# Kernel tuning notes

Measured on AMD Instinct MI355X. Metric: run time of the kernel, lower is better.

The kernel has to match this reference:

```python
import jax, jax.numpy as jnp
from jax import lax
import numpy as np

# 6D tensors: (N, C, h1, w1, h2, w2); weights: (Cout, Cin, k,k,k,k)
DN = lax.ConvDimensionNumbers(lhs_spec=(0, 1, 2, 3, 4, 5),
                              rhs_spec=(0, 1, 2, 3, 4, 5),
                              out_spec=(0, 1, 2, 3, 4, 5))


def conv4d_relu(x, w, b):
    # true 4D convolution, stride 1, SAME padding, then bias + ReLU
    y = lax.conv_general_dilated(x, w, window_strides=(1, 1, 1, 1),
                                 padding='SAME', dimension_numbers=DN)
    return jax.nn.relu(y + b.reshape(1, -1, 1, 1, 1, 1))


def _perm(x):
    # swap the two (h, w) spatial pairs of the correlation tensor
    return jnp.transpose(x, (0, 1, 4, 5, 2, 3))


def _sym(x, w, b):
    # symmetric_mode branch: f(x) + perm(f(perm(x)))
    return conv4d_relu(x, w, b) + _perm(conv4d_relu(_perm(x), w, b))


def setup_inputs() -> dict:
    key = jax.random.key(0)
    ks = jax.random.split(key, 9)
    B, S = 4, 20
    sc = 0.05
    return {
        'x':    jax.random.normal(ks[0], (B, 1, S, S, S, S), dtype=jnp.float32),
        'w0':   jax.random.normal(ks[1], (16, 1, 5, 5, 5, 5), dtype=jnp.float32) * sc,
        'b0':   jax.random.normal(ks[2], (16,), dtype=jnp.float32) * sc,
        'w10':  jax.random.normal(ks[3], (8, 16, 3, 3, 5, 5), dtype=jnp.float32) * sc,
        'b10':  jax.random.normal(ks[4], (8,), dtype=jnp.float32) * sc,
        'w11':  jax.random.normal(ks[5], (8, 16, 5, 5, 5, 5), dtype=jnp.float32) * sc,
        'b11':  jax.random.normal(ks[6], (8,), dtype=jnp.float32) * sc,
        'w2':   jax.random.normal(ks[7], (1, 16, 5, 5, 5, 5), dtype=jnp.float32) * sc,
        'b2':   jax.random.normal(ks[8], (1,), dtype=jnp.float32) * sc,
    }


def reference(x, w0, b0, w10, b10, w11, b11, w2, b2):
    x = _sym(x, w0, b0)                       # [B,16,S,S,S,S]
    x0 = _sym(x, w10, b10)                    # [B, 8,S,S,S,S]
    x1 = _sym(x, w11, b11)                    # [B, 8,S,S,S,S]
    x = jnp.concatenate((x0, x1), axis=1)     # [B,16,S,S,S,S]
    return _sym(x, w2, b2)                    # [B, 1,S,S,S,S]
```

## Files before the change

### kernel.cpp

```cpp
#include <hip/hip_runtime.h>

#define TS 20
#define TS2 400

typedef __attribute__((ext_vector_type(8))) __bf16 bf16x8;
typedef __attribute__((ext_vector_type(4))) __bf16 bf16x4;
typedef __attribute__((ext_vector_type(4))) float  f32x4;
typedef __attribute__((ext_vector_type(4))) int    int4v;

__device__ __forceinline__ float relu_f(float v) { return v > 0.0f ? v : 0.0f; }

#define MFMA16(a, b, c) __builtin_amdgcn_mfma_f32_16x16x32_bf16((a), (b), (c), 0, 0, 0)

#define LPAD 580

__global__ __launch_bounds__(256)
void pack_w0(const float* __restrict__ w0, __bf16* __restrict__ wpk0)
{
    int idx = blockIdx.x * 256 + (int)threadIdx.x;
    if (idx >= 25 * 32 * 32) return;
    const int c = idx & 31;
    const int m = (idx >> 5) & 31;
    const int e = idx >> 10;
    float v = 0.0f;
    if (c < 25) {
        const int co = m & 15;
        const int k1o = c / 5, k2o = c % 5, k3i = e / 5, k4i = e % 5;
        if (m < 16) v = w0[co * 625 + k1o * 125 + k2o * 25 + k3i * 5 + k4i];
        else        v = w0[co * 625 + k3i * 125 + k4i * 25 + k1o * 5 + k2o];
    }
    wpk0[idx] = (__bf16)v;
}

__global__ __launch_bounds__(256)
void pack_wmid(const float* __restrict__ w10, const float* __restrict__ w11,
               __bf16* __restrict__ wpk)
{
    int idx = blockIdx.x * 256 + (int)threadIdx.x;
    if (idx >= 650 * 512) return;
    const int ci  = idx & 15;
    const int m   = (idx >> 4) & 31;
    const int off = idx >> 9;
    const int inner = off % 26, outer = off / 26;
    const int d1 = outer / 5 - 2, d2 = outer % 5 - 2;
    float v = 0.0f;
    if (inner < 25) {
        const int d3 = inner / 5 - 2, d4 = inner % 5 - 2;
        const int co = m & 7;
        const bool isB  = (m & 8)  != 0;
        const bool is11 = (m & 16) != 0;
        if (is11) {
            int k1, k2, k3, k4;
            if (!isB) { k1 = d1 + 2; k2 = d2 + 2; k3 = d3 + 2; k4 = d4 + 2; }
            else      { k1 = d3 + 2; k2 = d4 + 2; k3 = d1 + 2; k4 = d2 + 2; }
            v = w11[((((co * 16 + ci) * 5 + k1) * 5 + k2) * 5 + k3) * 5 + k4];
        } else {
            if (!isB) {
                if (d1 >= -1 && d1 <= 1 && d2 >= -1 && d2 <= 1)
                    v = w10[((((co * 16 + ci) * 3 + (d1 + 1)) * 3 + (d2 + 1)) * 5 + (d3 + 2)) * 5 + (d4 + 2)];
            } else {
                if (d3 >= -1 && d3 <= 1 && d4 >= -1 && d4 <= 1)
                    v = w10[((((co * 16 + ci) * 3 + (d3 + 1)) * 3 + (d4 + 1)) * 5 + (d1 + 2)) * 5 + (d2 + 2)];
            }
        }
    }
    wpk[idx] = (__bf16)v;
}

__global__ __launch_bounds__(256)
void pack_w2f(const float* __restrict__ w2, __bf16* __restrict__ wpk2f)
{
    int idx = blockIdx.x * 256 + (int)threadIdx.x;
    if (idx >= 26 * 64 * 16) return;
    const int ci = idx & 15;
    const int m  = (idx >> 4) & 63;
    const int e  = idx >> 10;
    float v = 0.0f;
    if (e < 25) {
        if (m < 25)
            v = w2[ci * 625 + (m / 5) * 125 + (m % 5) * 25 + (e / 5) * 5 + (e % 5)];
        else if (m >= 32 && m < 57) {
            const int dd = m - 32;
            v = w2[ci * 625 + (e / 5) * 125 + (e % 5) * 25 + (dd / 5) * 5 + (dd % 5)];
        }
    }
    wpk2f[idx] = (__bf16)v;
}

__global__ __launch_bounds__(320)
void conv0_mfma(const float* __restrict__ x, const __bf16* __restrict__ wpk0,
                const float* __restrict__ b0, __bf16* __restrict__ y1)
{
    __shared__ __bf16 lds0[4 * LPAD * 8];

    const int tid  = (int)threadIdx.x;
    const int lane = tid & 63;
    const int wave = tid >> 6;
    const int bid  = blockIdx.x;
    const int o2 = bid % TS, o1 = (bid / TS) % TS, n = bid / TS2;

    for (int i = tid; i < 4 * LPAD * 8 / 2; i += 320) ((int*)lds0)[i] = 0;
    __syncthreads();

    for (int c = tid; c < 25 * TS2; c += 320) {
        const int pl = c / TS2, pt = c % TS2;
        const int i1 = o1 + pl / 5 - 2, i2 = o2 + pl % 5 - 2;
        if (i1 >= 0 && i1 < TS && i2 >= 0 && i2 < TS) {
            const float v = x[(size_t)((n * TS + i1) * TS + i2) * TS2 + pt];
            const int L = (pt / TS + 2) * 24 + (pt % TS + 2);
            lds0[((pl >> 3) * LPAD + L) * 8 + (pl & 7)] = (__bf16)v;
        }
    }
    __syncthreads();

    const int mrow = lane & 15;
    const int sub  = lane >> 4;

    int sb[5];
#pragma unroll
    for (int i = 0; i < 5; ++i) {
        const int p = (wave * 5 + i) * 16 + mrow;
        sb[i] = (sub * LPAD + (p / TS + 2) * 24 + (p % TS + 2)) * 8;
    }

    f32x4 acc0[5], acc1[5];
#pragma unroll
    for (int i = 0; i < 5; ++i) {
        acc0[i] = (f32x4){0.f, 0.f, 0.f, 0.f};
        acc1[i] = (f32x4){0.f, 0.f, 0.f, 0.f};
    }

    bf16x8 a0 = *(const bf16x8*)(wpk0 + (size_t)mrow * 32 + sub * 8);
    bf16x8 a1 = *(const bf16x8*)(wpk0 + (size_t)(16 + mrow) * 32 + sub * 8);
    for (int e = 0; e < 25; ++e) {
        bf16x8 na0 = a0, na1 = a1;
        if (e < 24) {
            na0 = *(const bf16x8*)(wpk0 + ((size_t)((e + 1) * 32 + mrow)) * 32 + sub * 8);
            na1 = *(const bf16x8*)(wpk0 + ((size_t)((e + 1) * 32 + 16 + mrow)) * 32 + sub * 8);
        }
        const int delta = ((e / 5 - 2) * 24 + (e % 5 - 2)) * 8;
#pragma unroll
        for (int i = 0; i < 5; ++i) {
            bf16x8 bfr = *(const bf16x8*)(&lds0[sb[i] + delta]);
            acc0[i] = MFMA16(a0, bfr, acc0[i]);
            acc1[i] = MFMA16(a1, bfr, acc1[i]);
        }
        a0 = na0; a1 = na1;
    }

    const f32x4 bv = *(const f32x4*)(b0 + sub * 4);
#pragma unroll
    for (int i = 0; i < 5; ++i) {
        const int p = (wave * 5 + i) * 16 + mrow;
        bf16x4 pk;
#pragma unroll
        for (int r = 0; r < 4; ++r)
            pk[r] = (__bf16)(relu_f(acc0[i][r] + bv[r]) + relu_f(acc1[i][r] + bv[r]));
        *(bf16x4*)(y1 + ((size_t)bid * TS2 + p) * 16 + sub * 4) = pk;
    }
}

__global__ __launch_bounds__(320)
void conv4d_mid_mfma(const __bf16* __restrict__ y1, const __bf16* __restrict__ wpk,
                     const float* __restrict__ b10, const float* __restrict__ b11,
                     __bf16* __restrict__ y2)
{
    __shared__ __bf16 lds[2][2 * LPAD * 8];

    const int tid  = (int)threadIdx.x;
    const int lane = tid & 63;
    const int wave = tid >> 6;
    const int bid0 = blockIdx.x;
    const int bid  = (bid0 & 7) * 200 + (bid0 >> 3);
    const int o2 = bid % TS, o1 = (bid / TS) % TS, n = bid / TS2;

    for (int i = tid; i < 2 * LPAD * 8; i += 320) ((int*)lds)[i] = 0;

    const int mrow = lane & 15;
    const int sub  = lane >> 4;
    const int aoff = (sub >> 1) * 512 + mrow * 16 + (sub & 1) * 8;

    int sbase[5];
#pragma unroll
    for (int i = 0; i < 5; ++i) {
        const int p  = (wave * 5 + i) * 16 + mrow;
        sbase[i] = ((sub & 1) * LPAD + (p / TS + 2) * 24 + (p % TS + 2)) * 8;
    }

    f32x4 acc[5][2];
#pragma unroll
    for (int i = 0; i < 5; ++i) {
        acc[i][0] = (f32x4){0.f, 0.f, 0.f, 0.f};
        acc[i][1] = (f32x4){0.f, 0.f, 0.f, 0.f};
    }

    __syncthreads();

    int buf = 0;
    for (int d1 = -2; d1 <= 2; ++d1) {
        const int i1 = o1 + d1;
        if (i1 < 0 || i1 >= TS) continue;
        for (int d2 = -2; d2 <= 2; ++d2) {
            const int i2 = o2 + d2;
            if (i2 < 0 || i2 >= TS) continue;

            const __bf16* src = y1 + (size_t)((n * TS + i1) * TS + i2) * TS2 * 16;
            for (int c = tid; c < 800; c += 320) {
                const int h = c / 40, rem = c % 40;
                const int w = rem >> 1, cb = rem & 1;
                int4v v = *(const int4v*)(src + c * 8);
                *(int4v*)(&lds[buf][(cb * LPAD + (h + 2) * 24 + 2 + w) * 8]) = v;
            }
            __syncthreads();

            const int outer = (d1 + 2) * 5 + (d2 + 2);
            const __bf16* wbase = wpk + (size_t)outer * 26 * 512;

            bf16x8 a0 = *(const bf16x8*)(wbase + aoff);
            bf16x8 a1 = *(const bf16x8*)(wbase + aoff + 256);
            for (int ic = 0; ic < 13; ++ic) {
                bf16x8 na0 = a0, na1 = a1;
                if (ic < 12) {
                    na0 = *(const bf16x8*)(wbase + (ic + 1) * 1024 + aoff);
                    na1 = *(const bf16x8*)(wbase + (ic + 1) * 1024 + aoff + 256);
                }
                const int e = 2 * ic + (sub >> 1);
                int d3 = 0, d4 = 0;
                if (e < 25) { d3 = e / 5 - 2; d4 = e % 5 - 2; }
                const int delta = (d3 * 24 + d4) * 8;
#pragma unroll
                for (int i = 0; i < 5; ++i) {
                    bf16x8 bfr = *(const bf16x8*)(&lds[buf][sbase[i] + delta]);
                    acc[i][0] = MFMA16(a0, bfr, acc[i][0]);
                    acc[i][1] = MFMA16(a1, bfr, acc[i][1]);
                }
                a0 = na0; a1 = na1;
            }
            buf ^= 1;
        }
    }

    const size_t base = (size_t)bid * TS2 * 16;
#pragma unroll
    for (int i = 0; i < 5; ++i) {
        const int p = (wave * 5 + i) * 16 + mrow;
#pragma unroll
        for (int mt = 0; mt < 2; ++mt) {
            const float* bs = mt ? b11 : b10;
            const f32x4 bv = *(const f32x4*)(bs + (sub & 1) * 4);
            bf16x4 pk;
#pragma unroll
            for (int r = 0; r < 4; ++r) {
                float v = relu_f(acc[i][mt][r] + bv[r]);
                float o = v + __shfl_xor(v, 32);
                pk[r] = (__bf16)o;
            }
            if (lane < 32)
                *(bf16x4*)(y2 + base + (size_t)p * 16 + mt * 8 + (sub & 1) * 4) = pk;
        }
    }
}

__global__ __launch_bounds__(320)
void conv2t_mfma(const __bf16* __restrict__ y2, const __bf16* __restrict__ wpk2f,
                 int n0, __bf16* __restrict__ t)
{
    __shared__ __bf16 lds[2 * LPAD * 8];

    const int tid  = (int)threadIdx.x;
    const int lane = tid & 63;
    const int wave = tid >> 6;
    const int bid = blockIdx.x;
    const int q2 = bid % TS, q1 = (bid / TS) % TS, nl = bid / TS2;

    for (int i = tid; i < 2 * LPAD * 8 / 2; i += 320) ((int*)lds)[i] = 0;
    __syncthreads();

    const __bf16* src = y2 + (size_t)(((n0 + nl) * TS + q1) * TS + q2) * TS2 * 16;
    for (int c = tid; c < 800; c += 320) {
        const int h = c / 40, rem = c % 40;
        const int w = rem >> 1, cb = rem & 1;
        int4v v = *(const int4v*)(src + c * 8);
        *(int4v*)(&lds[(cb * LPAD + (h + 2) * 24 + 2 + w) * 8]) = v;
    }
    __syncthreads();

    const int mrow = lane & 15;
    const int sub  = lane >> 4;

    int sbase[5];
#pragma unroll
    for (int i = 0; i < 5; ++i) {
        const int p  = (wave * 5 + i) * 16 + mrow;
        sbase[i] = ((sub & 1) * LPAD + (p / TS + 2) * 24 + (p % TS + 2)) * 8;
    }

    f32x4 acc[5][4];
#pragma unroll
    for (int i = 0; i < 5; ++i)
#pragma unroll
        for (int mt = 0; mt < 4; ++mt)
            acc[i][mt] = (f32x4){0.f, 0.f, 0.f, 0.f};

    for (int ic = 0; ic < 13; ++ic) {
        const int e = 2 * ic + (sub >> 1);
        int d3 = 0, d4 = 0;
        if (e < 25) { d3 = e / 5 - 2; d4 = e % 5 - 2; }
        const int delta = (d3 * 24 + d4) * 8;
        const __bf16* abase = wpk2f + ((size_t)e * 64 + mrow) * 16 + (sub & 1) * 8;
        bf16x8 a0 = *(const bf16x8*)(abase);
        bf16x8 a1 = *(const bf16x8*)(abase + 256);
        bf16x8 a2 = *(const bf16x8*)(abase + 512);
        bf16x8 a3 = *(const bf16x8*)(abase + 768);
#pragma unroll
        for (int i = 0; i < 5; ++i) {
            bf16x8 bfr = *(const bf16x8*)(&lds[sbase[i] + delta]);
            acc[i][0] = MFMA16(a0, bfr, acc[i][0]);
            acc[i][1] = MFMA16(a1, bfr, acc[i][1]);
            acc[i][2] = MFMA16(a2, bfr, acc[i][2]);
            acc[i][3] = MFMA16(a3, bfr, acc[i][3]);
        }
    }

    __bf16* tb = t + (size_t)((nl * TS + q1) * TS + q2) * (50 * TS2);
#pragma unroll
    for (int i = 0; i < 5; ++i) {
        const int p = (wave * 5 + i) * 16 + mrow;
#pragma unroll
        for (int mt = 0; mt < 4; ++mt) {
#pragma unroll
            for (int r = 0; r < 4; ++r) {
                const int gm = mt * 16 + sub * 4 + r;
                int m50 = -1;
                if (gm < 25) m50 = gm;
                else if (gm >= 32 && gm < 57) m50 = gm - 7;
                if (m50 >= 0) tb[m50 * TS2 + p] = (__bf16)acc[i][mt][r];
            }
        }
    }
}

__global__ __launch_bounds__(448)
void conv2_sum(const __bf16* __restrict__ t, const float* __restrict__ b2,
               int n0, float* __restrict__ out)
{
    const int tid = (int)threadIdx.x;
    if (tid >= TS2) return;
    const int bid = blockIdx.x;
    const int o2 = bid % TS, o1 = (bid / TS) % TS, nl = bid / TS2;

    float accA = 0.0f, accB = 0.0f;
    for (int dd = 0; dd < 25; ++dd) {
        const int q1 = o1 + dd / 5 - 2, q2 = o2 + dd % 5 - 2;
        if (q1 < 0 || q1 >= TS || q2 < 0 || q2 >= TS) continue;
        const __bf16* tb = t + (size_t)((nl * TS + q1) * TS + q2) * (50 * TS2) + tid;
        accA += (float)tb[dd * TS2];
        accB += (float)tb[(25 + dd) * TS2];
    }
    const float bias = b2[0];
    out[(size_t)(n0 + nl) * (TS2 * (size_t)TS2) + (size_t)(o1 * TS + o2) * TS2 + tid] =
        relu_f(accA + bias) + relu_f(accB + bias);
}

extern "C" void kernel_launch(void* const* d_in, const int* in_sizes, int n_in,
                              void* d_out, int out_size, void* d_ws, size_t ws_size,
                              hipStream_t stream)
{
    const float* x   = (const float*)d_in[0];
    const float* w0  = (const float*)d_in[1];
    const float* b0  = (const float*)d_in[2];
    const float* w10 = (const float*)d_in[3];
    const float* b10 = (const float*)d_in[4];
    const float* w11 = (const float*)d_in[5];
    const float* b11 = (const float*)d_in[6];
    const float* w2  = (const float*)d_in[7];
    const float* b2  = (const float*)d_in[8];
    float* out = (float*)d_out;

    __bf16* y1    = (__bf16*)d_ws;
    __bf16* y2    = y1 + (size_t)10240000;
    __bf16* tbuf  = y2 + (size_t)10240000;
    __bf16* wpkm  = tbuf + (size_t)16000000;
    __bf16* wpk0  = wpkm + 650 * 512;
    __bf16* wpk2f = wpk0 + 25 * 32 * 32;

    dim3 blk320(320), blk256(256), blk448(448);

    pack_w0  <<<dim3((25600 + 255) / 256),  blk256, 0, stream>>>(w0, wpk0);
    pack_wmid<<<dim3((332800 + 255) / 256), blk256, 0, stream>>>(w10, w11, wpkm);
    pack_w2f <<<dim3((26624 + 255) / 256),  blk256, 0, stream>>>(w2, wpk2f);

    conv0_mfma     <<<dim3(4 * TS * TS), blk320, 0, stream>>>(x, wpk0, b0, y1);
    conv4d_mid_mfma<<<dim3(1600),        blk320, 0, stream>>>(y1, wpkm, b10, b11, y2);

    for (int n0 = 0; n0 < 4; n0 += 2) {
        conv2t_mfma<<<dim3(800), blk320, 0, stream>>>(y2, wpk2f, n0, tbuf);
        conv2_sum  <<<dim3(800), blk448, 0, stream>>>(tbuf, b2, n0, out);
    }
}
```

Baseline: 494.0 us.

## Split mid-conv input channels into two halves to shrink LDS and repack weights

Changes the y1 layout so the 16 input channels are stored as two 8-channel halves, and the mid conv stages one half per step into a smaller LDS tile. Each K-step of 32 now covers four offsets with 8 channels instead of two offsets with 16, and the weights are repacked to match. LDS use drops, which may allow higher occupancy. In exchange there are twice as many barrier-separated stages, and the MFMA K padding changes from 26 to 28 offsets per half.

```diff
diff --git a/kernel.cpp b/kernel.cpp
--- a/kernel.cpp
+++ b/kernel.cpp
@@ -33,19 +33,24 @@
 }
 
 __global__ __launch_bounds__(256)
-void pack_wmid(const float* __restrict__ w10, const float* __restrict__ w11,
-               __bf16* __restrict__ wpk)
+void pack_wmid2(const float* __restrict__ w10, const float* __restrict__ w11,
+                __bf16* __restrict__ wpk)
 {
     int idx = blockIdx.x * 256 + (int)threadIdx.x;
-    if (idx >= 650 * 512) return;
-    const int ci  = idx & 15;
-    const int m   = (idx >> 4) & 31;
-    const int off = idx >> 9;
-    const int inner = off % 26, outer = off / 26;
+    if (idx >= 358400) return;
+    const int h     = idx / 179200;
+    int r           = idx % 179200;
+    const int outer = r / 7168;  r %= 7168;
+    const int ic    = r / 1024;  r %= 1024;
+    const int sub   = r / 256;   r %= 256;
+    const int m     = r / 8;
+    const int cil   = r % 8;
+    const int e  = 4 * ic + sub;
+    const int ci = h * 8 + cil;
     const int d1 = outer / 5 - 2, d2 = outer % 5 - 2;
     float v = 0.0f;
-    if (inner < 25) {
-        const int d3 = inner / 5 - 2, d4 = inner % 5 - 2;
+    if (e < 25) {
+        const int d3 = e / 5 - 2, d4 = e % 5 - 2;
         const int co = m & 7;
         const bool isB  = (m & 8)  != 0;
         const bool is11 = (m & 16) != 0;
@@ -156,7 +161,8 @@
 #pragma unroll
         for (int r = 0; r < 4; ++r)
             pk[r] = (__bf16)(relu_f(acc0[i][r] + bv[r]) + relu_f(acc1[i][r] + bv[r]));
-        *(bf16x4*)(y1 + ((size_t)bid * TS2 + p) * 16 + sub * 4) = pk;
+        *(bf16x4*)(y1 + (size_t)bid * 6400 + (size_t)(sub >> 1) * 3200
+                   + (size_t)p * 8 + (sub & 1) * 4) = pk;
     }
 }
 
@@ -165,7 +171,7 @@
                      const float* __restrict__ b10, const float* __restrict__ b11,
                      __bf16* __restrict__ y2)
 {
-    __shared__ __bf16 lds[2][2 * LPAD * 8];
+    __shared__ __bf16 lds[2][4608];
 
     const int tid  = (int)threadIdx.x;
     const int lane = tid & 63;
@@ -174,17 +180,17 @@
     const int bid  = (bid0 & 7) * 200 + (bid0 >> 3);
     const int o2 = bid % TS, o1 = (bid / TS) % TS, n = bid / TS2;
 
-    for (int i = tid; i < 2 * LPAD * 8; i += 320) ((int*)lds)[i] = 0;
+    for (int i = tid; i < 4608; i += 320) ((int*)lds)[i] = 0;
 
     const int mrow = lane & 15;
     const int sub  = lane >> 4;
-    const int aoff = (sub >> 1) * 512 + mrow * 16 + (sub & 1) * 8;
+    const int aoffc = sub * 256 + mrow * 8;
 
     int sbase[5];
 #pragma unroll
     for (int i = 0; i < 5; ++i) {
         const int p  = (wave * 5 + i) * 16 + mrow;
-        sbase[i] = ((sub & 1) * LPAD + (p / TS + 2) * 24 + (p % TS + 2)) * 8;
+        sbase[i] = ((p / TS + 2) * 24 + (p % TS + 2)) * 8;
     }
 
     f32x4 acc[5][2];
@@ -194,49 +200,62 @@
         acc[i][1] = (f32x4){0.f, 0.f, 0.f, 0.f};
     }
 
+    const __bf16* ybase = y1 + (size_t)n * TS2 * 6400;
+
     __syncthreads();
 
-    int buf = 0;
-    for (int d1 = -2; d1 <= 2; ++d1) {
-        const int i1 = o1 + d1;
-        if (i1 < 0 || i1 >= TS) continue;
-        for (int d2 = -2; d2 <= 2; ++d2) {
-            const int i2 = o2 + d2;
-            if (i2 < 0 || i2 >= TS) continue;
-
-            const __bf16* src = y1 + (size_t)((n * TS + i1) * TS + i2) * TS2 * 16;
-            for (int c = tid; c < 800; c += 320) {
-                const int h = c / 40, rem = c % 40;
-                const int w = rem >> 1, cb = rem & 1;
-                int4v v = *(const int4v*)(src + c * 8);
-                *(int4v*)(&lds[buf][(cb * LPAD + (h + 2) * 24 + 2 + w) * 8]) = v;
-            }
-            __syncthreads();
-
-            const int outer = (d1 + 2) * 5 + (d2 + 2);
-            const __bf16* wbase = wpk + (size_t)outer * 26 * 512;
-
-            bf16x8 a0 = *(const bf16x8*)(wbase + aoff);
-            bf16x8 a1 = *(const bf16x8*)(wbase + aoff + 256);
-            for (int ic = 0; ic < 13; ++ic) {
-                bf16x8 na0 = a0, na1 = a1;
-                if (ic < 12) {
-                    na0 = *(const bf16x8*)(wbase + (ic + 1) * 1024 + aoff);
-                    na1 = *(const bf16x8*)(wbase + (ic + 1) * 1024 + aoff + 256);
-                }
-                const int e = 2 * ic + (sub >> 1);
-                int d3 = 0, d4 = 0;
-                if (e < 25) { d3 = e / 5 - 2; d4 = e % 5 - 2; }
-                const int delta = (d3 * 24 + d4) * 8;
-#pragma unroll
-                for (int i = 0; i < 5; ++i) {
-                    bf16x8 bfr = *(const bf16x8*)(&lds[buf][sbase[i] + delta]);
-                    acc[i][0] = MFMA16(a0, bfr, acc[i][0]);
-                    acc[i][1] = MFMA16(a1, bfr, acc[i][1]);
-                }
-                a0 = na0; a1 = na1;
-            }
-            buf ^= 1;
+    int kk = 0;
+    {
+        while (kk < 25) {
+            const int i1 = o1 + kk / 5 - 2, i2 = o2 + kk % 5 - 2;
+            if (i1 >= 0 && i1 < TS && i2 >= 0 && i2 < TS) break;
+            ++kk;
+        }
+    }
+    int h = 0, buf = 0;
+    while (kk < 25) {
+        {
+            const __bf16* src = ybase
+                + (size_t)((o1 + kk / 5 - 2) * TS + (o2 + kk % 5 - 2)) * 6400
+                + (size_t)h * 3200;
+            for (int c = tid; c < 400; c += 320) {
+                const int dst = ((c / TS + 2) * 24 + (c % TS + 2)) * 8;
+                *(int4v*)(&lds[buf][dst]) = *(const int4v*)(src + c * 8);
+            }
+        }
+        __syncthreads();
+
+        const __bf16* wb = wpk + (size_t)(h * 25 + kk) * 7168;
+        bf16x8 a0 = *(const bf16x8*)(wb + aoffc);
+        bf16x8 a1 = *(const bf16x8*)(wb + aoffc + 128);
+        for (int ic = 0; ic < 7; ++ic) {
+            bf16x8 na0 = a0, na1 = a1;
+            if (ic < 6) {
+                na0 = *(const bf16x8*)(wb + (ic + 1) * 1024 + aoffc);
+                na1 = *(const bf16x8*)(wb + (ic + 1) * 1024 + aoffc + 128);
+            }
+            const int e = 4 * ic + sub;
+            int d3 = 0, d4 = 0;
+            if (e < 25) { d3 = e / 5 - 2; d4 = e % 5 - 2; }
+            const int delta = (d3 * 24 + d4) * 8;
+#pragma unroll
+            for (int i = 0; i < 5; ++i) {
+                bf16x8 bfr = *(const bf16x8*)(&lds[buf][sbase[i] + delta]);
+                acc[i][0] = MFMA16(a0, bfr, acc[i][0]);
+                acc[i][1] = MFMA16(a1, bfr, acc[i][1]);
+            }
+            a0 = na0; a1 = na1;
+        }
+
+        buf ^= 1;
+        if (++h == 2) {
+            h = 0;
+            ++kk;
+            while (kk < 25) {
+                const int i1 = o1 + kk / 5 - 2, i2 = o2 + kk % 5 - 2;
+                if (i1 >= 0 && i1 < TS && i2 >= 0 && i2 < TS) break;
+                ++kk;
+            }
         }
     }
 
@@ -381,14 +400,14 @@
     __bf16* y2    = y1 + (size_t)10240000;
     __bf16* tbuf  = y2 + (size_t)10240000;
     __bf16* wpkm  = tbuf + (size_t)16000000;
-    __bf16* wpk0  = wpkm + 650 * 512;
+    __bf16* wpk0  = wpkm + 358400;
     __bf16* wpk2f = wpk0 + 25 * 32 * 32;
 
     dim3 blk320(320), blk256(256), blk448(448);
 
-    pack_w0  <<<dim3((25600 + 255) / 256),  blk256, 0, stream>>>(w0, wpk0);
-    pack_wmid<<<dim3((332800 + 255) / 256), blk256, 0, stream>>>(w10, w11, wpkm);
-    pack_w2f <<<dim3((26624 + 255) / 256),  blk256, 0, stream>>>(w2, wpk2f);
+    pack_w0   <<<dim3((25600 + 255) / 256),  blk256, 0, stream>>>(w0, wpk0);
+    pack_wmid2<<<dim3((358400 + 255) / 256), blk256, 0, stream>>>(w10, w11, wpkm);
+    pack_w2f  <<<dim3((26624 + 255) / 256),  blk256, 0, stream>>>(w2, wpk2f);
 
     conv0_mfma     <<<dim3(4 * TS * TS), blk320, 0, stream>>>(x, wpk0, b0, y1);
     conv4d_mid_mfma<<<dim3(1600),        blk320, 0, stream>>>(y1, wpkm, b10, b11, y2);
```

Measured after the change: 504.1 us. 2.1% more time.
